# Kernel optimization log

Hardware: AMD Instinct MI355X
Metric: run time of the kernel (lower is better)

Reference implementation:

```python
import jax, jax.numpy as jnp
import numpy as np

N_NODES = 100000
N_EDGES = 1600000
N_REL = 8
IN_CH = 16
HID_CH = 32
OUT_CH = 2


def setup_inputs() -> dict:
    key = jax.random.key(0)
    ks = jax.random.split(key, 9)
    x = jax.random.normal(ks[0], (N_NODES, IN_CH), dtype=jnp.float32)
    edge_index = jax.random.randint(ks[1], (2, N_EDGES), 0, N_NODES, dtype=jnp.int64)
    edge_type = jax.random.randint(ks[2], (N_EDGES,), 0, N_REL, dtype=jnp.int64)
    s = 0.1
    W1 = jax.random.normal(ks[3], (N_REL, IN_CH, HID_CH), dtype=jnp.float32) * s
    root1 = jax.random.normal(ks[4], (IN_CH, HID_CH), dtype=jnp.float32) * s
    b1 = jnp.zeros((HID_CH,), dtype=jnp.float32)
    W2 = jax.random.normal(ks[5], (N_REL, HID_CH, OUT_CH), dtype=jnp.float32) * s
    root2 = jax.random.normal(ks[6], (HID_CH, OUT_CH), dtype=jnp.float32) * s
    b2 = jnp.zeros((OUT_CH,), dtype=jnp.float32)
    return {"x": x, "edge_index": edge_index, "edge_type": edge_type,
            "W1": W1, "root1": root1, "b1": b1,
            "W2": W2, "root2": root2, "b2": b2}


def rgcn_conv(x, W, Wroot, b, src, dst, rel, num_nodes, num_rel):
    """PyG RGCNConv: per-relation mean aggregation + root weight + bias."""
    # Transform all nodes by all relation weights up front: [N, R, H]
    xW = jnp.einsum('nf,rfh->nrh', x, W)
    msg = xW[src, rel]                       # [E, H] gather per edge
    # mean per (dst, relation): normalize each message by its group size
    key = dst * num_rel + rel                # combined segment key
    ones = jnp.ones(rel.shape, dtype=x.dtype)
    cnt = jax.ops.segment_sum(ones, key, num_segments=num_nodes * num_rel)
    norm = 1.0 / jnp.maximum(cnt, 1.0)
    msg = msg * norm[key][:, None]
    agg = jax.ops.segment_sum(msg, dst, num_segments=num_nodes)  # sum over relations
    return agg + x @ Wroot + b


def reference(x, edge_index, edge_type, W1, root1, b1, W2, root2, b2):
    src, dst = edge_index[0], edge_index[1]
    h = rgcn_conv(x, W1, root1, b1, src, dst, edge_type, N_NODES, N_REL)
    h = jax.nn.relu(h)
    # dropout is identity in eval mode (training=False)
    out = rgcn_conv(h, W2, root2, b2, src, dst, edge_type, N_NODES, N_REL)
    return jax.nn.log_softmax(out, axis=1)
```

## Files before the change

kernel.cpp:

```cpp
#include <hip/hip_runtime.h>
#include <math.h>

#define N_REL  8
#define IN_CH  16
#define HID_CH 32
#define OUT_CH 2

#define BIN_BITS  9
#define BIN_NODES 512
#define KPB       (BIN_NODES * N_REL)
#define NCHUNK    192
#define XW_TILE   64

static __device__ __forceinline__ unsigned short f2b(float f) {
    unsigned int u = __float_as_uint(f);
    u = (u + 0x7FFFu + ((u >> 16) & 1u)) >> 16;
    return (unsigned short)u;
}
static __device__ __forceinline__ float b2f(unsigned short s) {
    return __uint_as_float(((unsigned int)s) << 16);
}

__global__ __launch_bounds__(256) void prep_kernel(const float* __restrict__ x,
                                                   const float* __restrict__ W1,
                                                   unsigned short* __restrict__ xW16,
                                                   const int* __restrict__ dst,
                                                   int* __restrict__ H,
                                                   int N, int E, int nbins,
                                                   int chunksz, int nxw) {
    __shared__ float sx[XW_TILE * IN_CH];
    __shared__ int hist[256];
    int t = threadIdx.x;

    if ((int)blockIdx.x < nxw) {
        int node0 = blockIdx.x * XW_TILE;
        {
            int i4 = node0 * 4 + t;
            float4 v = make_float4(0.f, 0.f, 0.f, 0.f);
            if (i4 < N * 4) v = ((const float4*)x)[i4];
            ((float4*)sx)[t] = v;
        }
        __syncthreads();

        int r = t >> 5, c = t & 31;
        float w[IN_CH];
#pragma unroll
        for (int f = 0; f < IN_CH; ++f)
            w[f] = W1[(r * IN_CH + f) * HID_CH + c];

        int lim = N - node0; if (lim > XW_TILE) lim = XW_TILE;
        for (int ni = 0; ni < lim; ++ni) {
            const float4* xs = (const float4*)(sx + ni * IN_CH);
            float4 v0 = xs[0], v1 = xs[1], v2 = xs[2], v3 = xs[3];
            float a;
            a  = v0.x * w[0]  + v0.y * w[1]  + v0.z * w[2]  + v0.w * w[3];
            a += v1.x * w[4]  + v1.y * w[5]  + v1.z * w[6]  + v1.w * w[7];
            a += v2.x * w[8]  + v2.y * w[9]  + v2.z * w[10] + v2.w * w[11];
            a += v3.x * w[12] + v3.y * w[13] + v3.z * w[14] + v3.w * w[15];
            xW16[(node0 + ni) * (N_REL * HID_CH) + t] = f2b(a);
        }
    } else {
        int chunk = blockIdx.x - nxw;
        int e0 = chunk * chunksz;
        int e1 = e0 + chunksz; if (e1 > E) e1 = E;

        for (int i = t; i < nbins; i += 256) hist[i] = 0;
        __syncthreads();
        for (int e = e0 + t; e < e1; e += 256)
            atomicAdd(&hist[dst[e] >> BIN_BITS], 1);
        __syncthreads();
        for (int i = t; i < nbins; i += 256)
            H[i * NCHUNK + chunk] = hist[i];
    }
}

__global__ __launch_bounds__(1024) void scan_a_kernel(int* __restrict__ ptr,
                                                      int* __restrict__ blksum, int M) {
    int i = blockIdx.x * 1024 + threadIdx.x;
    int val = (i < M) ? ptr[i] : 0;
    int lane = threadIdx.x & 63;
    int wid  = threadIdx.x >> 6;

    int v = val;
#pragma unroll
    for (int off = 1; off < 64; off <<= 1) {
        int u = __shfl_up(v, off, 64);
        if (lane >= off) v += u;
    }

    __shared__ int wsum[16];
    if (lane == 63) wsum[wid] = v;
    __syncthreads();

    if (wid == 0) {
        int worig = (lane < 16) ? wsum[lane] : 0;
        int wv = worig;
#pragma unroll
        for (int off = 1; off < 16; off <<= 1) {
            int u = __shfl_up(wv, off, 64);
            if (lane >= off) wv += u;
        }
        if (lane < 16) wsum[lane] = wv - worig;
        if (lane == 15) blksum[blockIdx.x] = wv;
    }
    __syncthreads();

    if (i < M) ptr[i] = (v - val) + wsum[wid];
}

__global__ void scan_b_kernel(int* __restrict__ blksum, int nb) {
    int lane = threadIdx.x & 63;
    int run = 0;
    for (int base = 0; base < nb; base += 64) {
        int i = base + lane;
        int val = (i < nb) ? blksum[i] : 0;
        int v = val;
#pragma unroll
        for (int off = 1; off < 64; off <<= 1) {
            int u = __shfl_up(v, off, 64);
            if (lane >= off) v += u;
        }
        if (i < nb) blksum[i] = run + (v - val);
        run += __shfl(v, 63, 64);
    }
}

__global__ __launch_bounds__(256) void part_scatter_kernel(const int* __restrict__ src,
                                                           const int* __restrict__ dst,
                                                           const int* __restrict__ rel,
                                                           const int* __restrict__ Hs,
                                                           const int* __restrict__ blksum,
                                                           int* __restrict__ be,
                                                           int E, int nbins, int chunksz) {
    __shared__ int base[256];
    __shared__ int fil[256];
    int chunk = blockIdx.x;
    int e0 = chunk * chunksz;
    int e1 = e0 + chunksz; if (e1 > E) e1 = E;

    for (int i = threadIdx.x; i < nbins; i += 256) {
        int idx = i * NCHUNK + chunk;
        base[i] = Hs[idx] + blksum[idx >> 10];
        fil[i]  = 0;
    }
    __syncthreads();

    for (int e = e0 + threadIdx.x; e < e1; e += 256) {
        int d = dst[e];
        int b = d >> BIN_BITS;
        int slot = base[b] + atomicAdd(&fil[b], 1);
        be[slot] = ((d & (BIN_NODES - 1)) << 20) | (rel[e] << 17) | src[e];
    }
}

__global__ __launch_bounds__(256) void bin_build_kernel(const int* __restrict__ be,
                                                        const int* __restrict__ Hs,
                                                        const int* __restrict__ blksum,
                                                        int* __restrict__ rowptr,
                                                        int* __restrict__ csr,
                                                        float* __restrict__ einv,
                                                        int E, int nbins) {
    int b  = blockIdx.x;
    int i0 = b * NCHUNK;
    int s0 = Hs[i0] + blksum[i0 >> 10];
    int s1 = E;
    if (b + 1 < nbins) {
        int i1 = (b + 1) * NCHUNK;
        s1 = Hs[i1] + blksum[i1 >> 10];
    }
    int t  = threadIdx.x;

    __shared__ int cnt[KPB];
    __shared__ int off[KPB];
    __shared__ int fil[KPB];
    __shared__ int ws[4];

    for (int i = t; i < KPB; i += 256) { cnt[i] = 0; fil[i] = 0; }
    __syncthreads();

    for (int p = s0 + t; p < s1; p += 256)
        atomicAdd(&cnt[be[p] >> 17], 1);
    __syncthreads();

    int kbase = t * 16;
    int loc[16];
    int sum = 0;
#pragma unroll
    for (int i = 0; i < 16; ++i) { loc[i] = sum; sum += cnt[kbase + i]; }

    int lane = t & 63, wid = t >> 6;
    int v = sum;
#pragma unroll
    for (int o = 1; o < 64; o <<= 1) {
        int u = __shfl_up(v, o, 64);
        if (lane >= o) v += u;
    }
    if (lane == 63) ws[wid] = v;
    __syncthreads();
    int woff = 0;
    for (int i = 0; i < wid; ++i) woff += ws[i];
    int excl = woff + (v - sum);
#pragma unroll
    for (int i = 0; i < 16; ++i) off[kbase + i] = excl + loc[i];
    __syncthreads();

    for (int i = t; i < KPB; i += 256)
        if ((i & 7) == 7)
            rowptr[b * BIN_NODES + (i >> 3) + 1] = s0 + off[i] + cnt[i];
    if (b == 0 && t == 0) rowptr[0] = 0;

    for (int p = s0 + t; p < s1; p += 256) {
        int pk = be[p];
        int k  = pk >> 17;
        int slot = s0 + off[k] + atomicAdd(&fil[k], 1);
        csr[slot]  = ((pk & 0x1FFFF) << 3) | (k & 7);
        einv[slot] = 1.0f / (float)cnt[k];
    }
}

#define STAGE_SW2(sw2, W2, root2)                                              \
    for (int i = threadIdx.x; i < 288; i += 256) {                             \
        int f = i / 9, j = i - f * 9;                                          \
        float a, bb;                                                           \
        if (j < 8) { a = W2[(j * HID_CH + f) * 2]; bb = W2[(j * HID_CH + f) * 2 + 1]; } \
        else       { a = root2[f * 2];             bb = root2[f * 2 + 1]; }    \
        sw2[i] = make_float2(a, bb);                                           \
    }

#define EPILOGUE_V2(sw2, hval, node, c, hW16, hroot, b2)                       \
    {                                                                          \
        int g  = (c >> 4) << 4;                                                \
        int jj = c & 15; if (jj > 8) jj = 8;                                   \
        float o0 = 0.0f, o1 = 0.0f;                                            \
        _Pragma("unroll")                                                      \
        for (int k = 0; k < 16; ++k) {                                         \
            float hf = __shfl(hval, g + k, 32);                                \
            float2 wv = sw2[(g + k) * 9 + jj];                                 \
            o0 = fmaf(hf, wv.x, o0);                                           \
            o1 = fmaf(hf, wv.y, o1);                                           \
        }                                                                      \
        o0 += __shfl_xor(o0, 16, 32);                                          \
        o1 += __shfl_xor(o1, 16, 32);                                          \
        if (c < 8) {                                                           \
            hW16[((node) << 3) + c] = ((unsigned)f2b(o1) << 16) | f2b(o0);     \
        } else if (c == 8) {                                                   \
            *(float2*)(hroot + ((long)(node) << 1)) =                          \
                make_float2(o0 + b2[0], o1 + b2[1]);                           \
        }                                                                      \
    }

__global__ __launch_bounds__(256) void l1_fused_kernel(const float* __restrict__ x,
                                                       const int* __restrict__ csr,
                                                       const float* __restrict__ einv,
                                                       const int* __restrict__ rowptr,
                                                       const unsigned short* __restrict__ xW16,
                                                       const float* __restrict__ root1,
                                                       const float* __restrict__ b1,
                                                       const float* __restrict__ W2,
                                                       const float* __restrict__ root2,
                                                       const float* __restrict__ b2,
                                                       unsigned int* __restrict__ hW16,
                                                       float* __restrict__ hroot, int N) {
    __shared__ float2 sw2[32 * 9];
    STAGE_SW2(sw2, W2, root2)
    __syncthreads();

    int gid  = blockIdx.x * 256 + threadIdx.x;
    int node = gid >> 5;
    int c    = gid & 31;
    if (node >= N) return;

    int p0 = __ldg(&rowptr[node]);
    int p1 = __ldg(&rowptr[node + 1]);

    float acc0 = 0.0f, acc1 = 0.0f;
    int p = p0;
    for (; p + 7 < p1; p += 8) {
        int v0 = csr[p],     v1 = csr[p + 1], v2 = csr[p + 2], v3 = csr[p + 3];
        int v4 = csr[p + 4], v5 = csr[p + 5], v6 = csr[p + 6], v7 = csr[p + 7];
        float i0 = einv[p],     i1 = einv[p + 1], i2 = einv[p + 2], i3 = einv[p + 3];
        float i4 = einv[p + 4], i5 = einv[p + 5], i6 = einv[p + 6], i7 = einv[p + 7];
        float a0 = b2f(xW16[(v0 << 5) + c]);
        float a1 = b2f(xW16[(v1 << 5) + c]);
        float a2 = b2f(xW16[(v2 << 5) + c]);
        float a3 = b2f(xW16[(v3 << 5) + c]);
        float a4 = b2f(xW16[(v4 << 5) + c]);
        float a5 = b2f(xW16[(v5 << 5) + c]);
        float a6 = b2f(xW16[(v6 << 5) + c]);
        float a7 = b2f(xW16[(v7 << 5) + c]);
        acc0 = fmaf(a0, i0, acc0);
        acc1 = fmaf(a1, i1, acc1);
        acc0 = fmaf(a2, i2, acc0);
        acc1 = fmaf(a3, i3, acc1);
        acc0 = fmaf(a4, i4, acc0);
        acc1 = fmaf(a5, i5, acc1);
        acc0 = fmaf(a6, i6, acc0);
        acc1 = fmaf(a7, i7, acc1);
    }
    for (; p + 3 < p1; p += 4) {
        int v0 = csr[p], v1 = csr[p + 1], v2 = csr[p + 2], v3 = csr[p + 3];
        float i0 = einv[p], i1 = einv[p + 1], i2 = einv[p + 2], i3 = einv[p + 3];
        acc0 = fmaf(b2f(xW16[(v0 << 5) + c]), i0, acc0);
        acc1 = fmaf(b2f(xW16[(v1 << 5) + c]), i1, acc1);
        acc0 = fmaf(b2f(xW16[(v2 << 5) + c]), i2, acc0);
        acc1 = fmaf(b2f(xW16[(v3 << 5) + c]), i3, acc1);
    }
    if (p + 1 < p1) {
        int v0 = csr[p], v1 = csr[p + 1];
        acc0 = fmaf(b2f(xW16[(v0 << 5) + c]), einv[p], acc0);
        acc1 = fmaf(b2f(xW16[(v1 << 5) + c]), einv[p + 1], acc1);
        p += 2;
    }
    if (p < p1)
        acc0 = fmaf(b2f(xW16[(csr[p] << 5) + c]), einv[p], acc0);

    const float4* xs = (const float4*)(x + ((long)node << 4));
    float4 v0 = xs[0], v1 = xs[1], v2 = xs[2], v3 = xs[3];
    const float* wr = root1 + c;
    float acc = acc0 + acc1 + b1[c];
    acc += v0.x * wr[0]   + v0.y * wr[32]  + v0.z * wr[64]  + v0.w * wr[96];
    acc += v1.x * wr[128] + v1.y * wr[160] + v1.z * wr[192] + v1.w * wr[224];
    acc += v2.x * wr[256] + v2.y * wr[288] + v2.z * wr[320] + v2.w * wr[352];
    acc += v3.x * wr[384] + v3.y * wr[416] + v3.z * wr[448] + v3.w * wr[480];
    float hval = fmaxf(acc, 0.0f);

    EPILOGUE_V2(sw2, hval, node, c, hW16, hroot, b2)
}

__global__ __launch_bounds__(256) void l1_fb_kernel(const float* __restrict__ x,
                                                    const int* __restrict__ csr,
                                                    const float* __restrict__ einv,
                                                    const int* __restrict__ rowptr,
                                                    const float* __restrict__ W1,
                                                    const float* __restrict__ root1,
                                                    const float* __restrict__ b1,
                                                    const float* __restrict__ W2,
                                                    const float* __restrict__ root2,
                                                    const float* __restrict__ b2,
                                                    unsigned int* __restrict__ hW16,
                                                    float* __restrict__ hroot, int N) {
    __shared__ float sW[N_REL * IN_CH * HID_CH];
    __shared__ float2 sw2[32 * 9];
    for (int i = threadIdx.x; i < N_REL * IN_CH * HID_CH; i += 256) sW[i] = W1[i];
    STAGE_SW2(sw2, W2, root2)
    __syncthreads();

    int gid  = blockIdx.x * 256 + threadIdx.x;
    int node = gid >> 5;
    int c    = gid & 31;
    if (node >= N) return;

    int p0 = __ldg(&rowptr[node]);
    int p1 = __ldg(&rowptr[node + 1]);

    float acc = 0.0f;
    for (int p = p0; p < p1; ++p) {
        int v = csr[p];
        int s = v >> 3, r = v & 7;
        const float4* xsv = (const float4*)(x + ((long)s << 4));
        float4 q0 = xsv[0], q1 = xsv[1], q2 = xsv[2], q3 = xsv[3];
        const float* w = sW + ((r * IN_CH) * HID_CH) + c;
        float a;
        a  = q0.x * w[0]   + q0.y * w[32]  + q0.z * w[64]  + q0.w * w[96];
        a += q1.x * w[128] + q1.y * w[160] + q1.z * w[192] + q1.w * w[224];
        a += q2.x * w[256] + q2.y * w[288] + q2.z * w[320] + q2.w * w[352];
        a += q3.x * w[384] + q3.y * w[416] + q3.z * w[448] + q3.w * w[480];
        acc = fmaf(a, einv[p], acc);
    }

    const float4* xs = (const float4*)(x + ((long)node << 4));
    float4 v0 = xs[0], v1 = xs[1], v2 = xs[2], v3 = xs[3];
    const float* wr = root1 + c;
    acc += b1[c];
    acc += v0.x * wr[0]   + v0.y * wr[32]  + v0.z * wr[64]  + v0.w * wr[96];
    acc += v1.x * wr[128] + v1.y * wr[160] + v1.z * wr[192] + v1.w * wr[224];
    acc += v2.x * wr[256] + v2.y * wr[288] + v2.z * wr[320] + v2.w * wr[352];
    acc += v3.x * wr[384] + v3.y * wr[416] + v3.z * wr[448] + v3.w * wr[480];
    float hval = fmaxf(acc, 0.0f);

    EPILOGUE_V2(sw2, hval, node, c, hW16, hroot, b2)
}

__global__ __launch_bounds__(256) void l2_flat_kernel(const int* __restrict__ csr,
                                                      const float* __restrict__ einv,
                                                      const int* __restrict__ rowptr,
                                                      const unsigned int* __restrict__ hW16,
                                                      const float* __restrict__ hroot,
                                                      float* __restrict__ out, int N) {
    int gid  = blockIdx.x * 256 + threadIdx.x;
    int node = gid >> 4;
    int l    = gid & 15;
    if (node >= N) return;

    int p0 = __ldg(&rowptr[node]);
    int p1 = __ldg(&rowptr[node + 1]);

    float o0 = 0.0f, o1 = 0.0f;
    for (int p = p0 + l; p < p1; p += 16) {
        int v = csr[p];
        float w = einv[p];
        unsigned u = hW16[v];
        o0 = fmaf(b2f((unsigned short)u), w, o0);
        o1 = fmaf(b2f((unsigned short)(u >> 16)), w, o1);
    }

#pragma unroll
    for (int m = 1; m < 16; m <<= 1) {
        o0 += __shfl_xor(o0, m, 64);
        o1 += __shfl_xor(o1, m, 64);
    }

    if (l == 0) {
        float2 rt = *(const float2*)(hroot + ((long)node << 1));
        o0 += rt.x; o1 += rt.y;
        float mx = fmaxf(o0, o1);
        float lg = mx + logf(__expf(o0 - mx) + __expf(o1 - mx));
        *(float2*)(out + ((long)node << 1)) = make_float2(o0 - lg, o1 - lg);
    }
}

extern "C" void kernel_launch(void* const* d_in, const int* in_sizes, int n_in,
                              void* d_out, int out_size, void* d_ws, size_t ws_size,
                              hipStream_t stream) {
    const float* x     = (const float*)d_in[0];
    const int*   eidx  = (const int*)d_in[1];
    const int*   etype = (const int*)d_in[2];
    const float* W1    = (const float*)d_in[3];
    const float* root1 = (const float*)d_in[4];
    const float* b1    = (const float*)d_in[5];
    const float* W2    = (const float*)d_in[6];
    const float* root2 = (const float*)d_in[7];
    const float* b2    = (const float*)d_in[8];
    float* out = (float*)d_out;

    const int N = in_sizes[0] / IN_CH;
    const int E = in_sizes[2];
    const int nbins   = (N + BIN_NODES - 1) >> BIN_BITS;
    const int chunksz = (E + NCHUNK - 1) / NCHUNK;
    const int M2      = nbins * NCHUNK;
    const int* src = eidx;
    const int* dst = eidx + E;

    char* wp = (char*)d_ws;
    auto take = [&](size_t bytes) {
        char* p = wp;
        wp += (bytes + 63) & ~(size_t)63;
        return p;
    };
    int*   H      = (int*)take((size_t)M2 * sizeof(int));
    int*   blksum = (int*)take(4096 * sizeof(int));
    int*   rowptr = (int*)take((size_t)(nbins * BIN_NODES + 1) * sizeof(int));
    int*   csr    = (int*)take((size_t)E * sizeof(int));
    float* einv   = (float*)take((size_t)E * sizeof(float));
    int*   be     = (int*)take((size_t)E * sizeof(int));
    unsigned int* hW16 = (unsigned int*)take((size_t)N * N_REL * sizeof(unsigned int));
    float* hroot  = (float*)take((size_t)N * 2 * sizeof(float));
    unsigned short* xW16 = (unsigned short*)take((size_t)N * N_REL * HID_CH * sizeof(unsigned short));
    bool use_xw = ((size_t)(wp - (char*)d_ws) <= ws_size);

    const int B = 256;
    const int nb = (M2 + 1023) / 1024;
    const int nxw = use_xw ? (N + XW_TILE - 1) / XW_TILE : 0;

    prep_kernel<<<nxw + NCHUNK, B, 0, stream>>>(x, W1, xW16, dst, H, N, E, nbins, chunksz, nxw);
    scan_a_kernel<<<nb, 1024, 0, stream>>>(H, blksum, M2);
    scan_b_kernel<<<1, 64, 0, stream>>>(blksum, nb);
    part_scatter_kernel<<<NCHUNK, B, 0, stream>>>(src, dst, etype, H, blksum, be, E, nbins, chunksz);
    bin_build_kernel<<<nbins, B, 0, stream>>>(be, H, blksum, rowptr, csr, einv, E, nbins);

    if (use_xw) {
        l1_fused_kernel<<<(N * 32 + B - 1) / B, B, 0, stream>>>(
            x, csr, einv, rowptr, xW16, root1, b1, W2, root2, b2, hW16, hroot, N);
    } else {
        l1_fb_kernel<<<(N * 32 + B - 1) / B, B, 0, stream>>>(
            x, csr, einv, rowptr, W1, root1, b1, W2, root2, b2, hW16, hroot, N);
    }

    l2_flat_kernel<<<(N * 16 + B - 1) / B, B, 0, stream>>>(csr, einv, rowptr, hW16, hroot, out, N);
}
```

Baseline: 152.9 us.

## Fold histogram scan into scatter kernel and pack csr/einv into int2

Removes the two separate scan kernels: each part_scatter block now redundantly sums the per-bin histogram rows and runs a shared-memory block scan to compute its bin bases, with chunk 0 writing bin start offsets for bin_build. The csr index and inverse-count arrays are interleaved into a single int2 array, so the aggregation kernels fetch both with one 8-byte load. NCHUNK rises from 192 to 256 to widen the histogram/scatter grid. This cuts two launches and some separate memory streams, at the cost of redundant per-block row summation over nbins×NCHUNK entries.

```diff
diff --git a/kernel.cpp b/kernel.cpp
--- a/kernel.cpp
+++ b/kernel.cpp
@@ -9,7 +9,7 @@
 #define BIN_BITS  9
 #define BIN_NODES 512
 #define KPB       (BIN_NODES * N_REL)
-#define NCHUNK    192
+#define NCHUNK    256
 #define XW_TILE   64
 
 static __device__ __forceinline__ unsigned short f2b(float f) {
@@ -74,78 +74,46 @@
     }
 }
 
-__global__ __launch_bounds__(1024) void scan_a_kernel(int* __restrict__ ptr,
-                                                      int* __restrict__ blksum, int M) {
-    int i = blockIdx.x * 1024 + threadIdx.x;
-    int val = (i < M) ? ptr[i] : 0;
-    int lane = threadIdx.x & 63;
-    int wid  = threadIdx.x >> 6;
-
-    int v = val;
-#pragma unroll
-    for (int off = 1; off < 64; off <<= 1) {
-        int u = __shfl_up(v, off, 64);
-        if (lane >= off) v += u;
-    }
-
-    __shared__ int wsum[16];
-    if (lane == 63) wsum[wid] = v;
-    __syncthreads();
-
-    if (wid == 0) {
-        int worig = (lane < 16) ? wsum[lane] : 0;
-        int wv = worig;
-#pragma unroll
-        for (int off = 1; off < 16; off <<= 1) {
-            int u = __shfl_up(wv, off, 64);
-            if (lane >= off) wv += u;
-        }
-        if (lane < 16) wsum[lane] = wv - worig;
-        if (lane == 15) blksum[blockIdx.x] = wv;
-    }
-    __syncthreads();
-
-    if (i < M) ptr[i] = (v - val) + wsum[wid];
-}
-
-__global__ void scan_b_kernel(int* __restrict__ blksum, int nb) {
-    int lane = threadIdx.x & 63;
-    int run = 0;
-    for (int base = 0; base < nb; base += 64) {
-        int i = base + lane;
-        int val = (i < nb) ? blksum[i] : 0;
-        int v = val;
-#pragma unroll
-        for (int off = 1; off < 64; off <<= 1) {
-            int u = __shfl_up(v, off, 64);
-            if (lane >= off) v += u;
-        }
-        if (i < nb) blksum[i] = run + (v - val);
-        run += __shfl(v, 63, 64);
-    }
-}
-
 __global__ __launch_bounds__(256) void part_scatter_kernel(const int* __restrict__ src,
                                                            const int* __restrict__ dst,
                                                            const int* __restrict__ rel,
-                                                           const int* __restrict__ Hs,
-                                                           const int* __restrict__ blksum,
+                                                           const int* __restrict__ H,
+                                                           int* __restrict__ binstart,
                                                            int* __restrict__ be,
                                                            int E, int nbins, int chunksz) {
     __shared__ int base[256];
+    __shared__ int scanbuf[256];
     __shared__ int fil[256];
     int chunk = blockIdx.x;
+    int i = threadIdx.x;
     int e0 = chunk * chunksz;
     int e1 = e0 + chunksz; if (e1 > E) e1 = E;
 
-    for (int i = threadIdx.x; i < nbins; i += 256) {
-        int idx = i * NCHUNK + chunk;
-        base[i] = Hs[idx] + blksum[idx >> 10];
-        fil[i]  = 0;
-    }
-    __syncthreads();
-
-    for (int e = e0 + threadIdx.x; e < e1; e += 256) {
+    int mypre = 0, mytot = 0;
+    if (i < nbins) {
+        const int* row = H + i * NCHUNK;
+        for (int ch = 0; ch < NCHUNK; ++ch) {
+            int v = row[ch];
+            mytot += v;
+            if (ch < chunk) mypre += v;
+        }
+    }
+    scanbuf[i] = mytot;
+    __syncthreads();
+#pragma unroll
+    for (int d = 1; d < 256; d <<= 1) {
+        int add = (i >= d) ? scanbuf[i - d] : 0;
+        __syncthreads();
+        scanbuf[i] += add;
+        __syncthreads();
+    }
+    int excl = scanbuf[i] - mytot;
+    base[i] = excl + mypre;
+    fil[i]  = 0;
+    if (chunk == 0 && i <= nbins) binstart[i] = excl;
+    __syncthreads();
+
+    for (int e = e0 + i; e < e1; e += 256) {
         int d = dst[e];
         int b = d >> BIN_BITS;
         int slot = base[b] + atomicAdd(&fil[b], 1);
@@ -154,20 +122,13 @@
 }
 
 __global__ __launch_bounds__(256) void bin_build_kernel(const int* __restrict__ be,
-                                                        const int* __restrict__ Hs,
-                                                        const int* __restrict__ blksum,
+                                                        const int* __restrict__ binstart,
                                                         int* __restrict__ rowptr,
-                                                        int* __restrict__ csr,
-                                                        float* __restrict__ einv,
+                                                        int2* __restrict__ ce,
                                                         int E, int nbins) {
     int b  = blockIdx.x;
-    int i0 = b * NCHUNK;
-    int s0 = Hs[i0] + blksum[i0 >> 10];
-    int s1 = E;
-    if (b + 1 < nbins) {
-        int i1 = (b + 1) * NCHUNK;
-        s1 = Hs[i1] + blksum[i1 >> 10];
-    }
+    int s0 = binstart[b];
+    int s1 = binstart[b + 1];
     int t  = threadIdx.x;
 
     __shared__ int cnt[KPB];
@@ -213,8 +174,8 @@
         int pk = be[p];
         int k  = pk >> 17;
         int slot = s0 + off[k] + atomicAdd(&fil[k], 1);
-        csr[slot]  = ((pk & 0x1FFFF) << 3) | (k & 7);
-        einv[slot] = 1.0f / (float)cnt[k];
+        ce[slot] = make_int2(((pk & 0x1FFFF) << 3) | (k & 7),
+                             __float_as_int(1.0f / (float)cnt[k]));
     }
 }
 
@@ -250,8 +211,7 @@
     }
 
 __global__ __launch_bounds__(256) void l1_fused_kernel(const float* __restrict__ x,
-                                                       const int* __restrict__ csr,
-                                                       const float* __restrict__ einv,
+                                                       const int2* __restrict__ ce,
                                                        const int* __restrict__ rowptr,
                                                        const unsigned short* __restrict__ xW16,
                                                        const float* __restrict__ root1,
@@ -276,43 +236,42 @@
     float acc0 = 0.0f, acc1 = 0.0f;
     int p = p0;
     for (; p + 7 < p1; p += 8) {
-        int v0 = csr[p],     v1 = csr[p + 1], v2 = csr[p + 2], v3 = csr[p + 3];
-        int v4 = csr[p + 4], v5 = csr[p + 5], v6 = csr[p + 6], v7 = csr[p + 7];
-        float i0 = einv[p],     i1 = einv[p + 1], i2 = einv[p + 2], i3 = einv[p + 3];
-        float i4 = einv[p + 4], i5 = einv[p + 5], i6 = einv[p + 6], i7 = einv[p + 7];
-        float a0 = b2f(xW16[(v0 << 5) + c]);
-        float a1 = b2f(xW16[(v1 << 5) + c]);
-        float a2 = b2f(xW16[(v2 << 5) + c]);
-        float a3 = b2f(xW16[(v3 << 5) + c]);
-        float a4 = b2f(xW16[(v4 << 5) + c]);
-        float a5 = b2f(xW16[(v5 << 5) + c]);
-        float a6 = b2f(xW16[(v6 << 5) + c]);
-        float a7 = b2f(xW16[(v7 << 5) + c]);
-        acc0 = fmaf(a0, i0, acc0);
-        acc1 = fmaf(a1, i1, acc1);
-        acc0 = fmaf(a2, i2, acc0);
-        acc1 = fmaf(a3, i3, acc1);
-        acc0 = fmaf(a4, i4, acc0);
-        acc1 = fmaf(a5, i5, acc1);
-        acc0 = fmaf(a6, i6, acc0);
-        acc1 = fmaf(a7, i7, acc1);
+        int2 e0 = ce[p],     e1 = ce[p + 1], e2 = ce[p + 2], e3 = ce[p + 3];
+        int2 e4 = ce[p + 4], e5 = ce[p + 5], e6 = ce[p + 6], e7 = ce[p + 7];
+        float a0 = b2f(xW16[(e0.x << 5) + c]);
+        float a1 = b2f(xW16[(e1.x << 5) + c]);
+        float a2 = b2f(xW16[(e2.x << 5) + c]);
+        float a3 = b2f(xW16[(e3.x << 5) + c]);
+        float a4 = b2f(xW16[(e4.x << 5) + c]);
+        float a5 = b2f(xW16[(e5.x << 5) + c]);
+        float a6 = b2f(xW16[(e6.x << 5) + c]);
+        float a7 = b2f(xW16[(e7.x << 5) + c]);
+        acc0 = fmaf(a0, __int_as_float(e0.y), acc0);
+        acc1 = fmaf(a1, __int_as_float(e1.y), acc1);
+        acc0 = fmaf(a2, __int_as_float(e2.y), acc0);
+        acc1 = fmaf(a3, __int_as_float(e3.y), acc1);
+        acc0 = fmaf(a4, __int_as_float(e4.y), acc0);
+        acc1 = fmaf(a5, __int_as_float(e5.y), acc1);
+        acc0 = fmaf(a6, __int_as_float(e6.y), acc0);
+        acc1 = fmaf(a7, __int_as_float(e7.y), acc1);
     }
     for (; p + 3 < p1; p += 4) {
-        int v0 = csr[p], v1 = csr[p + 1], v2 = csr[p + 2], v3 = csr[p + 3];
-        float i0 = einv[p], i1 = einv[p + 1], i2 = einv[p + 2], i3 = einv[p + 3];
-        acc0 = fmaf(b2f(xW16[(v0 << 5) + c]), i0, acc0);
-        acc1 = fmaf(b2f(xW16[(v1 << 5) + c]), i1, acc1);
-        acc0 = fmaf(b2f(xW16[(v2 << 5) + c]), i2, acc0);
-        acc1 = fmaf(b2f(xW16[(v3 << 5) + c]), i3, acc1);
+        int2 e0 = ce[p], e1 = ce[p + 1], e2 = ce[p + 2], e3 = ce[p + 3];
+        acc0 = fmaf(b2f(xW16[(e0.x << 5) + c]), __int_as_float(e0.y), acc0);
+        acc1 = fmaf(b2f(xW16[(e1.x << 5) + c]), __int_as_float(e1.y), acc1);
+        acc0 = fmaf(b2f(xW16[(e2.x << 5) + c]), __int_as_float(e2.y), acc0);
+        acc1 = fmaf(b2f(xW16[(e3.x << 5) + c]), __int_as_float(e3.y), acc1);
     }
     if (p + 1 < p1) {
-        int v0 = csr[p], v1 = csr[p + 1];
-        acc0 = fmaf(b2f(xW16[(v0 << 5) + c]), einv[p], acc0);
-        acc1 = fmaf(b2f(xW16[(v1 << 5) + c]), einv[p + 1], acc1);
+        int2 e0 = ce[p], e1 = ce[p + 1];
+        acc0 = fmaf(b2f(xW16[(e0.x << 5) + c]), __int_as_float(e0.y), acc0);
+        acc1 = fmaf(b2f(xW16[(e1.x << 5) + c]), __int_as_float(e1.y), acc1);
         p += 2;
     }
-    if (p < p1)
-        acc0 = fmaf(b2f(xW16[(csr[p] << 5) + c]), einv[p], acc0);
+    if (p < p1) {
+        int2 e0 = ce[p];
+        acc0 = fmaf(b2f(xW16[(e0.x << 5) + c]), __int_as_float(e0.y), acc0);
+    }
 
     const float4* xs = (const float4*)(x + ((long)node << 4));
     float4 v0 = xs[0], v1 = xs[1], v2 = xs[2], v3 = xs[3];
@@ -328,8 +287,7 @@
 }
 
 __global__ __launch_bounds__(256) void l1_fb_kernel(const float* __restrict__ x,
-                                                    const int* __restrict__ csr,
-                                                    const float* __restrict__ einv,
+                                                    const int2* __restrict__ ce,
                                                     const int* __restrict__ rowptr,
                                                     const float* __restrict__ W1,
                                                     const float* __restrict__ root1,
@@ -355,8 +313,8 @@
 
     float acc = 0.0f;
     for (int p = p0; p < p1; ++p) {
-        int v = csr[p];
-        int s = v >> 3, r = v & 7;
+        int2 e = ce[p];
+        int s = e.x >> 3, r = e.x & 7;
         const float4* xsv = (const float4*)(x + ((long)s << 4));
         float4 q0 = xsv[0], q1 = xsv[1], q2 = xsv[2], q3 = xsv[3];
         const float* w = sW + ((r * IN_CH) * HID_CH) + c;
@@ -365,7 +323,7 @@
         a += q1.x * w[128] + q1.y * w[160] + q1.z * w[192] + q1.w * w[224];
         a += q2.x * w[256] + q2.y * w[288] + q2.z * w[320] + q2.w * w[352];
         a += q3.x * w[384] + q3.y * w[416] + q3.z * w[448] + q3.w * w[480];
-        acc = fmaf(a, einv[p], acc);
+        acc = fmaf(a, __int_as_float(e.y), acc);
     }
 
     const float4* xs = (const float4*)(x + ((long)node << 4));
@@ -381,8 +339,7 @@
     EPILOGUE_V2(sw2, hval, node, c, hW16, hroot, b2)
 }
 
-__global__ __launch_bounds__(256) void l2_flat_kernel(const int* __restrict__ csr,
-                                                      const float* __restrict__ einv,
+__global__ __launch_bounds__(256) void l2_flat_kernel(const int2* __restrict__ ce,
                                                       const int* __restrict__ rowptr,
                                                       const unsigned int* __restrict__ hW16,
                                                       const float* __restrict__ hroot,
@@ -397,9 +354,9 @@
 
     float o0 = 0.0f, o1 = 0.0f;
     for (int p = p0 + l; p < p1; p += 16) {
-        int v = csr[p];
-        float w = einv[p];
-        unsigned u = hW16[v];
+        int2 e = ce[p];
+        float w = __int_as_float(e.y);
+        unsigned u = hW16[e.x];
         o0 = fmaf(b2f((unsigned short)u), w, o0);
         o1 = fmaf(b2f((unsigned short)(u >> 16)), w, o1);
     }
@@ -447,34 +404,30 @@
         wp += (bytes + 63) & ~(size_t)63;
         return p;
     };
-    int*   H      = (int*)take((size_t)M2 * sizeof(int));
-    int*   blksum = (int*)take(4096 * sizeof(int));
-    int*   rowptr = (int*)take((size_t)(nbins * BIN_NODES + 1) * sizeof(int));
-    int*   csr    = (int*)take((size_t)E * sizeof(int));
-    float* einv   = (float*)take((size_t)E * sizeof(float));
-    int*   be     = (int*)take((size_t)E * sizeof(int));
+    int*   H        = (int*)take((size_t)M2 * sizeof(int));
+    int*   binstart = (int*)take(512 * sizeof(int));
+    int*   rowptr   = (int*)take((size_t)(nbins * BIN_NODES + 1) * sizeof(int));
+    int2*  ce       = (int2*)take((size_t)E * sizeof(int2));
+    int*   be       = (int*)take((size_t)E * sizeof(int));
     unsigned int* hW16 = (unsigned int*)take((size_t)N * N_REL * sizeof(unsigned int));
-    float* hroot  = (float*)take((size_t)N * 2 * sizeof(float));
+    float* hroot    = (float*)take((size_t)N * 2 * sizeof(float));
     unsigned short* xW16 = (unsigned short*)take((size_t)N * N_REL * HID_CH * sizeof(unsigned short));
     bool use_xw = ((size_t)(wp - (char*)d_ws) <= ws_size);
 
     const int B = 256;
-    const int nb = (M2 + 1023) / 1024;
     const int nxw = use_xw ? (N + XW_TILE - 1) / XW_TILE : 0;
 
     prep_kernel<<<nxw + NCHUNK, B, 0, stream>>>(x, W1, xW16, dst, H, N, E, nbins, chunksz, nxw);
-    scan_a_kernel<<<nb, 1024, 0, stream>>>(H, blksum, M2);
-    scan_b_kernel<<<1, 64, 0, stream>>>(blksum, nb);
-    part_scatter_kernel<<<NCHUNK, B, 0, stream>>>(src, dst, etype, H, blksum, be, E, nbins, chunksz);
-    bin_build_kernel<<<nbins, B, 0, stream>>>(be, H, blksum, rowptr, csr, einv, E, nbins);
+    part_scatter_kernel<<<NCHUNK, B, 0, stream>>>(src, dst, etype, H, binstart, be, E, nbins, chunksz);
+    bin_build_kernel<<<nbins, B, 0, stream>>>(be, binstart, rowptr, ce, E, nbins);
 
     if (use_xw) {
         l1_fused_kernel<<<(N * 32 + B - 1) / B, B, 0, stream>>>(
-            x, csr, einv, rowptr, xW16, root1, b1, W2, root2, b2, hW16, hroot, N);
+            x, ce, rowptr, xW16, root1, b1, W2, root2, b2, hW16, hroot, N);
     } else {
         l1_fb_kernel<<<(N * 32 + B - 1) / B, B, 0, stream>>>(
-            x, csr, einv, rowptr, W1, root1, b1, W2, root2, b2, hW16, hroot, N);
-    }
-
-    l2_flat_kernel<<<(N * 16 + B - 1) / B, B, 0, stream>>>(csr, einv, rowptr, hW16, hroot, out, N);
-}
+            x, ce, rowptr, W1, root1, b1, W2, root2, b2, hW16, hroot, N);
+    }
+
+    l2_flat_kernel<<<(N * 16 + B - 1) / B, B, 0, stream>>>(ce, rowptr, hW16, hroot, out, N);
+}
```

Result: no change. 150.6 us (-1.5%).
